# Kernel optimization log

Measured on AMD Instinct MI355X. Metric: run time of the kernel, lower is better.

Reference implementation:

```python
import jax, jax.numpy as jnp
import numpy as np

EPS = 1e-8

def quaternion_normalize(q):
    # q: [..., 4] -> unit quaternion
    return q / (jnp.linalg.norm(q, axis=-1, keepdims=True) + EPS)

def quaternion_mul(q1, q2):
    # Hamilton product; q1, q2 broadcastable [..., 4]
    w1, x1, y1, z1 = q1[..., 0], q1[..., 1], q1[..., 2], q1[..., 3]
    w2, x2, y2, z2 = q2[..., 0], q2[..., 1], q2[..., 2], q2[..., 3]
    w = w1 * w2 - x1 * x2 - y1 * y2 - z1 * z2
    x = w1 * x2 + x1 * w2 + y1 * z2 - z1 * y2
    y = w1 * y2 - x1 * z2 + y1 * w2 + z1 * x2
    z = w1 * z2 + x1 * y2 - y1 * x2 + z1 * w2
    return jnp.stack([w, x, y, z], axis=-1)

def setup_inputs() -> dict:
    key = jax.random.key(0)
    ks = jax.random.split(key, 7)
    B, N, M, D = 2, 512, 512, 256
    return {
        "vision_feat": jax.random.normal(ks[0], (B, N, D), dtype=jnp.float32),
        "text_feat": jax.random.normal(ks[1], (B, M, D), dtype=jnp.float32),
        "Wv": jax.random.normal(ks[2], (D, D), dtype=jnp.float32) * (1.0 / np.sqrt(D)),
        "bv": jax.random.normal(ks[3], (D,), dtype=jnp.float32) * 0.01,
        "Wt": jax.random.normal(ks[4], (D, D), dtype=jnp.float32) * (1.0 / np.sqrt(D)),
        "bt": jax.random.normal(ks[5], (D,), dtype=jnp.float32) * 0.01,
        "h": jnp.float32(1.0),
    }

def reference(vision_feat, text_feat, Wv, bv, Wt, bt, h):
    B, N, D = vision_feat.shape
    M = text_feat.shape[1]
    heads = D // 4
    # project to spinors and normalize per-quaternion
    v_spinor = quaternion_normalize((vision_feat @ Wv.T + bv).reshape(B, N, heads, 4))
    t_spinor = quaternion_normalize((text_feat @ Wt.T + bt).reshape(B, M, heads, 4))
    # broadcast pairwise quaternion product v * conj(t): [B, N, M, heads, 4]
    v_exp = v_spinor[:, :, None]                      # [B, N, 1, heads, 4]
    t_conj = t_spinor[:, None, :] * jnp.array([1.0, -1.0, -1.0, -1.0], dtype=t_spinor.dtype)
    inner = quaternion_mul(v_exp, t_conj)             # [B, N, M, heads, 4]
    vec_norm = jnp.linalg.norm(inner[..., 1:], axis=-1)
    w = inner[..., 0]
    gamma = 2.0 * jnp.arctan2(vec_norm, w + EPS)
    interference = jnp.cos(gamma / 2.0) ** 2          # [B, N, M, heads]
    attn = jax.nn.softmax(interference.mean(axis=-1) / jnp.sqrt(jnp.float32(D)), axis=-1)  # [B, N, M]
    new_vision = jnp.matmul(attn, text_feat)                      # [B, N, D]
    new_text = jnp.matmul(attn.transpose(0, 2, 1), vision_feat)   # [B, M, D]
    out_vision = vision_feat + h * new_vision
    out_text = text_feat + h * new_text
    return (out_vision, out_text)
```

## Files before the change

### kernel.cpp

```cpp
#include <hip/hip_runtime.h>
#include <math.h>

#define EPS 1e-8f

typedef short bf16x8 __attribute__((ext_vector_type(8)));
typedef short bf16x4 __attribute__((ext_vector_type(4)));
typedef float f32x4  __attribute__((ext_vector_type(4)));

__device__ __forceinline__ short f2bf(float f) {
    union { float fv; unsigned u; } v; v.fv = f;
    unsigned r = v.u + 0x7fffu + ((v.u >> 16) & 1u);
    return (short)(r >> 16);
}
__device__ __forceinline__ float bf2f(short s) {
    union { unsigned u; float f; } v;
    v.u = ((unsigned)(unsigned short)s) << 16;
    return v.f;
}
__device__ __forceinline__ bf16x8 pack8(float4 a, float4 b) {
    bf16x8 p;
    p[0] = f2bf(a.x); p[1] = f2bf(a.y); p[2] = f2bf(a.z); p[3] = f2bf(a.w);
    p[4] = f2bf(b.x); p[5] = f2bf(b.y); p[6] = f2bf(b.z); p[7] = f2bf(b.w);
    return p;
}

__global__ __launch_bounds__(256) void proj_expand_kernel(
    const float* __restrict__ vis, const float* __restrict__ txt,
    const float* __restrict__ Wv, const float* __restrict__ bv,
    const float* __restrict__ Wt, const float* __restrict__ bt,
    short* __restrict__ expq)
{
    const int which = blockIdx.z;
    const float* X    = which == 0 ? vis : txt;
    const float* W    = which == 0 ? Wv : Wt;
    const float* bias = which == 0 ? bv : bt;
    short* Eo = expq + which * 1024 * 1024;

    const int r0 = blockIdx.x * 32;
    const int c0 = blockIdx.y * 64;
    const int t = threadIdx.x, lane = t & 63, wave = t >> 6;
    const int wr = (wave >> 1) * 16, wc = (wave & 1) * 32;
    const int mrow = lane & 15, quad = lane >> 4;

    __shared__ __align__(16) short As[32][72];
    __shared__ __align__(16) short Bs[64][72];

    f32x4 acc[2] = {};

    const int srow = t >> 3, skg = t & 7;
    for (int k0 = 0; k0 < 256; k0 += 64) {
        const float* xp = X + (r0 + srow) * 256 + k0 + 8 * skg;
        float4 xa = *(const float4*)xp, xb = *(const float4*)(xp + 4);
        const float* wp0 = W + (c0 + srow) * 256 + k0 + 8 * skg;
        const float* wp1 = W + (c0 + srow + 32) * 256 + k0 + 8 * skg;
        float4 wa0 = *(const float4*)wp0, wb0 = *(const float4*)(wp0 + 4);
        float4 wa1 = *(const float4*)wp1, wb1 = *(const float4*)(wp1 + 4);
        __syncthreads();
        *(bf16x8*)&As[srow][8 * skg]      = pack8(xa, xb);
        *(bf16x8*)&Bs[srow][8 * skg]      = pack8(wa0, wb0);
        *(bf16x8*)&Bs[srow + 32][8 * skg] = pack8(wa1, wb1);
        __syncthreads();
        #pragma unroll
        for (int kh = 0; kh < 2; ++kh) {
            bf16x8 a  = *(bf16x8*)&As[wr + mrow][32 * kh + 8 * quad];
            bf16x8 b0 = *(bf16x8*)&Bs[wc + mrow][32 * kh + 8 * quad];
            bf16x8 b1 = *(bf16x8*)&Bs[wc + 16 + mrow][32 * kh + 8 * quad];
            acc[0] = __builtin_amdgcn_mfma_f32_16x16x32_bf16(a, b0, acc[0], 0, 0, 0);
            acc[1] = __builtin_amdgcn_mfma_f32_16x16x32_bf16(a, b1, acc[1], 0, 0, 0);
        }
    }

    const int qbase = lane & ~3;
    #pragma unroll
    for (int j = 0; j < 2; ++j) {
        const int col  = c0 + wc + 16 * j + mrow;
        const float bb = bias[col];
        const int head = col >> 2;
        #pragma unroll
        for (int reg = 0; reg < 4; ++reg) {
            const int row = r0 + wr + quad * 4 + reg;
            float v = acc[j][reg] + bb;
            float s = v * v;
            s += __shfl_xor(s, 1, 64);
            s += __shfl_xor(s, 2, 64);
            float q = v * (1.f / (sqrtf(s) + EPS));
            float q0 = __shfl(q, qbase + 0, 64);
            float q1 = __shfl(q, qbase + 1, 64);
            float q2 = __shfl(q, qbase + 2, 64);
            float q3 = __shfl(q, qbase + 3, 64);
            bf16x4 p;
            p[0] = f2bf(q * q0); p[1] = f2bf(q * q1);
            p[2] = f2bf(q * q2); p[3] = f2bf(q * q3);
            *(bf16x4*)(Eo + row * 1024 + head * 16 + (col & 3) * 4) = p;
        }
    }
}

__global__ __launch_bounds__(256) void logits_kernel(
    const short* __restrict__ expq, short* __restrict__ E,
    float* __restrict__ rs)
{
    const int b  = blockIdx.z;
    const int r0 = blockIdx.x * 32;
    const int c0 = blockIdx.y * 64;
    const int t = threadIdx.x, lane = t & 63, wave = t >> 6;
    const int wr = (wave >> 1) * 16, wc = (wave & 1) * 32;
    const int mrow = lane & 15, quad = lane >> 4;

    __shared__ __align__(16) short As[32][72];
    __shared__ __align__(16) short Bs[64][72];

    const short* Abase = expq + (b * 512 + r0) * 1024;
    const short* Bbase = expq + (1024 + b * 512 + c0) * 1024;

    f32x4 acc[2] = {};
    const int srow = t >> 3, skg = t & 7;
    for (int k0 = 0; k0 < 1024; k0 += 64) {
        bf16x8 av = *(const bf16x8*)(Abase + srow * 1024 + k0 + 8 * skg);
        bf16x8 b0v = *(const bf16x8*)(Bbase + srow * 1024 + k0 + 8 * skg);
        bf16x8 b1v = *(const bf16x8*)(Bbase + (srow + 32) * 1024 + k0 + 8 * skg);
        __syncthreads();
        *(bf16x8*)&As[srow][8 * skg]      = av;
        *(bf16x8*)&Bs[srow][8 * skg]      = b0v;
        *(bf16x8*)&Bs[srow + 32][8 * skg] = b1v;
        __syncthreads();
        #pragma unroll
        for (int kh = 0; kh < 2; ++kh) {
            bf16x8 a  = *(bf16x8*)&As[wr + mrow][32 * kh + 8 * quad];
            bf16x8 b0 = *(bf16x8*)&Bs[wc + mrow][32 * kh + 8 * quad];
            bf16x8 b1 = *(bf16x8*)&Bs[wc + 16 + mrow][32 * kh + 8 * quad];
            acc[0] = __builtin_amdgcn_mfma_f32_16x16x32_bf16(a, b0, acc[0], 0, 0, 0);
            acc[1] = __builtin_amdgcn_mfma_f32_16x16x32_bf16(a, b1, acc[1], 0, 0, 0);
        }
    }

    float e[2][4];
    #pragma unroll
    for (int j = 0; j < 2; ++j)
        #pragma unroll
        for (int reg = 0; reg < 4; ++reg)
            e[j][reg] = __expf(acc[j][reg] * (1.f / 1024.f));

    #pragma unroll
    for (int j = 0; j < 2; ++j) {
        const int col = c0 + wc + 16 * j + mrow;
        #pragma unroll
        for (int reg = 0; reg < 4; ++reg) {
            const int row = r0 + wr + quad * 4 + reg;
            E[(b * 512 + row) * 512 + col] = f2bf(e[j][reg]);
        }
    }
    #pragma unroll
    for (int reg = 0; reg < 4; ++reg) {
        float p = e[0][reg] + e[1][reg];
        p += __shfl_xor(p, 1, 64);
        p += __shfl_xor(p, 2, 64);
        p += __shfl_xor(p, 4, 64);
        p += __shfl_xor(p, 8, 64);
        if (mrow == 0) {
            const int row = r0 + wr + quad * 4 + reg;
            rs[(b * 512 + row) * 16 + (c0 >> 5) + (wc >> 5)] = p;
        }
    }
}

__global__ __launch_bounds__(256) void out_kernel(
    const float* __restrict__ vis, const float* __restrict__ txt,
    const short* __restrict__ E, const float* __restrict__ rs,
    const float* __restrict__ hptr,
    float* __restrict__ outv, float* __restrict__ outt)
{
    const int z = blockIdx.z;
    const int b = z & 1, which = z >> 1;
    const int r0 = blockIdx.x * 32;
    const int c0 = blockIdx.y * 64;
    const int t = threadIdx.x, lane = t & 63, wave = t >> 6;
    const int wr = (wave >> 1) * 16, wc = (wave & 1) * 32;
    const int mrow = lane & 15, quad = lane >> 4;
    const float hv = hptr[0];

    const short* Eb   = E + b * 512 * 512;
    const float* S    = (which == 0 ? txt : vis) + b * 512 * 256;
    const float* base = (which == 0 ? vis : txt) + b * 512 * 256;
    float*       out  = (which == 0 ? outv : outt) + b * 512 * 256;

    __shared__ __align__(16) short As[32][72];
    __shared__ __align__(16) short Bs[64][72];
    __shared__ float rinv_s[512];

    #pragma unroll
    for (int u = 0; u < 2; ++u) {
        const int row = t + 256 * u;
        const float* p = rs + (b * 512 + row) * 16;
        float s = 0.f;
        #pragma unroll
        for (int i = 0; i < 16; ++i) s += p[i];
        rinv_s[row] = 1.f / s;
    }
    __syncthreads();

    f32x4 acc[2] = {};
    const int kkB = t >> 3, cg = t & 7;
    const int rowA = t >> 3, kgA = t & 7;
    const int nnA = t >> 2, mgA = t & 3;

    for (int k0 = 0; k0 < 512; k0 += 64) {
        float4 sa[2], sb[2];
        #pragma unroll
        for (int u = 0; u < 2; ++u) {
            const float* sp = S + (k0 + kkB + 32 * u) * 256 + c0 + 8 * cg;
            sa[u] = *(const float4*)sp; sb[u] = *(const float4*)(sp + 4);
        }
        bf16x8 arow;
        float af[8];
        if (which == 0) {
            arow = *(const bf16x8*)(Eb + (r0 + rowA) * 512 + k0 + 8 * kgA);
        } else {
            bf16x8 ev = *(const bf16x8*)(Eb + (k0 + nnA) * 512 + r0 + 8 * mgA);
            const float ri = rinv_s[k0 + nnA];
            #pragma unroll
            for (int c = 0; c < 8; ++c) af[c] = bf2f(ev[c]) * ri;
        }
        __syncthreads();
        if (which == 0) {
            *(bf16x8*)&As[rowA][8 * kgA] = arow;
        } else {
            #pragma unroll
            for (int c = 0; c < 8; ++c) As[8 * mgA + c][nnA] = f2bf(af[c]);
        }
        #pragma unroll
        for (int u = 0; u < 2; ++u) {
            const int kk = kkB + 32 * u;
            Bs[8 * cg + 0][kk] = f2bf(sa[u].x);
            Bs[8 * cg + 1][kk] = f2bf(sa[u].y);
            Bs[8 * cg + 2][kk] = f2bf(sa[u].z);
            Bs[8 * cg + 3][kk] = f2bf(sa[u].w);
            Bs[8 * cg + 4][kk] = f2bf(sb[u].x);
            Bs[8 * cg + 5][kk] = f2bf(sb[u].y);
            Bs[8 * cg + 6][kk] = f2bf(sb[u].z);
            Bs[8 * cg + 7][kk] = f2bf(sb[u].w);
        }
        __syncthreads();
        #pragma unroll
        for (int kh = 0; kh < 2; ++kh) {
            bf16x8 a  = *(bf16x8*)&As[wr + mrow][32 * kh + 8 * quad];
            bf16x8 b0 = *(bf16x8*)&Bs[wc + mrow][32 * kh + 8 * quad];
            bf16x8 b1 = *(bf16x8*)&Bs[wc + 16 + mrow][32 * kh + 8 * quad];
            acc[0] = __builtin_amdgcn_mfma_f32_16x16x32_bf16(a, b0, acc[0], 0, 0, 0);
            acc[1] = __builtin_amdgcn_mfma_f32_16x16x32_bf16(a, b1, acc[1], 0, 0, 0);
        }
    }

    #pragma unroll
    for (int j = 0; j < 2; ++j) {
        const int col = c0 + wc + 16 * j + mrow;
        #pragma unroll
        for (int reg = 0; reg < 4; ++reg) {
            const int row = r0 + wr + quad * 4 + reg;
            const float scale = which == 0 ? hv * rinv_s[row] : hv;
            out[row * 256 + col] = fmaf(scale, acc[j][reg], base[row * 256 + col]);
        }
    }
}

extern "C" void kernel_launch(void* const* d_in, const int* in_sizes, int n_in,
                              void* d_out, int out_size, void* d_ws, size_t ws_size,
                              hipStream_t stream)
{
    const float* vis = (const float*)d_in[0];
    const float* txt = (const float*)d_in[1];
    const float* Wv  = (const float*)d_in[2];
    const float* bv  = (const float*)d_in[3];
    const float* Wt  = (const float*)d_in[4];
    const float* bt  = (const float*)d_in[5];
    const float* h   = (const float*)d_in[6];

    float* outv = (float*)d_out;
    float* outt = (float*)d_out + 2 * 512 * 256;

    short* expq = (short*)d_ws;
    short* E    = expq + 2048 * 1024;
    float* rs   = (float*)(E + 1024 * 512);

    proj_expand_kernel<<<dim3(32, 4, 2), 256, 0, stream>>>(vis, txt, Wv, bv, Wt, bt, expq);
    logits_kernel<<<dim3(16, 8, 2), 256, 0, stream>>>(expq, E, rs);
    out_kernel<<<dim3(16, 4, 4), 256, 0, stream>>>(vis, txt, E, rs, h, outv, outt);
}
```

Before: 94.09 us.

## Emit transposed bf16 features in projection kernel; restage expansion epilogue via LDS

The projection kernel now writes a transposed bf16 copy of each input feature tile (taken from its shared-memory A tile) into workspace. The output kernel can then load its B operand with vectorized bf16 loads instead of reading fp32, converting and doing scalar transposed LDS stores. The quaternion outer-product epilogue is also rewritten to stage accumulators through LDS and emit two 16-byte stores per head instead of shuffles and 8-byte stores. This adds workspace traffic and an extra barrier in the projection kernel.

```diff
diff --git a/kernel.cpp b/kernel.cpp
--- a/kernel.cpp
+++ b/kernel.cpp
@@ -4,7 +4,6 @@
 #define EPS 1e-8f
 
 typedef short bf16x8 __attribute__((ext_vector_type(8)));
-typedef short bf16x4 __attribute__((ext_vector_type(4)));
 typedef float f32x4  __attribute__((ext_vector_type(4)));
 
 __device__ __forceinline__ short f2bf(float f) {
@@ -28,7 +27,7 @@
     const float* __restrict__ vis, const float* __restrict__ txt,
     const float* __restrict__ Wv, const float* __restrict__ bv,
     const float* __restrict__ Wt, const float* __restrict__ bt,
-    short* __restrict__ expq)
+    short* __restrict__ expq, short* __restrict__ St)
 {
     const int which = blockIdx.z;
     const float* X    = which == 0 ? vis : txt;
@@ -48,6 +47,8 @@
     f32x4 acc[2] = {};
 
     const int srow = t >> 3, skg = t & 7;
+    const int kexp = 64 * blockIdx.y;
+
     for (int k0 = 0; k0 < 256; k0 += 64) {
         const float* xp = X + (r0 + srow) * 256 + k0 + 8 * skg;
         float4 xa = *(const float4*)xp, xb = *(const float4*)(xp + 4);
@@ -68,31 +69,52 @@
             acc[0] = __builtin_amdgcn_mfma_f32_16x16x32_bf16(a, b0, acc[0], 0, 0, 0);
             acc[1] = __builtin_amdgcn_mfma_f32_16x16x32_bf16(a, b1, acc[1], 0, 0, 0);
         }
-    }
-
-    const int qbase = lane & ~3;
+        if (k0 == kexp) {
+            const int kk = t & 63, rg = t >> 6;
+            bf16x8 p;
+            #pragma unroll
+            for (int i = 0; i < 8; ++i) p[i] = As[8 * rg + i][kk];
+            const int b = r0 >> 9, mb = r0 & 511;
+            *(bf16x8*)(St + which * 262144 + b * 131072 +
+                       (kexp + kk) * 512 + mb + 8 * rg) = p;
+        }
+    }
+
+    __syncthreads();
+    float* fs = (float*)&Bs[0][0];
     #pragma unroll
     for (int j = 0; j < 2; ++j) {
-        const int col  = c0 + wc + 16 * j + mrow;
-        const float bb = bias[col];
-        const int head = col >> 2;
+        const int lcol = wc + 16 * j + mrow;
+        const float bb = bias[c0 + lcol];
         #pragma unroll
         for (int reg = 0; reg < 4; ++reg) {
-            const int row = r0 + wr + quad * 4 + reg;
-            float v = acc[j][reg] + bb;
-            float s = v * v;
-            s += __shfl_xor(s, 1, 64);
-            s += __shfl_xor(s, 2, 64);
-            float q = v * (1.f / (sqrtf(s) + EPS));
-            float q0 = __shfl(q, qbase + 0, 64);
-            float q1 = __shfl(q, qbase + 1, 64);
-            float q2 = __shfl(q, qbase + 2, 64);
-            float q3 = __shfl(q, qbase + 3, 64);
-            bf16x4 p;
-            p[0] = f2bf(q * q0); p[1] = f2bf(q * q1);
-            p[2] = f2bf(q * q2); p[3] = f2bf(q * q3);
-            *(bf16x4*)(Eo + row * 1024 + head * 16 + (col & 3) * 4) = p;
-        }
+            const int lrow = wr + quad * 4 + reg;
+            fs[lrow * 65 + lcol] = acc[j][reg] + bb;
+        }
+    }
+    __syncthreads();
+    #pragma unroll
+    for (int u = 0; u < 2; ++u) {
+        const int qid = t + 256 * u;
+        const int lrow = qid >> 4, lhq = qid & 15;
+        const float* qp = fs + lrow * 65 + 4 * lhq;
+        float q0 = qp[0], q1 = qp[1], q2 = qp[2], q3 = qp[3];
+        float s = q0 * q0 + q1 * q1 + q2 * q2 + q3 * q3;
+        float inv = 1.f / (sqrtf(s) + EPS);
+        q0 *= inv; q1 *= inv; q2 *= inv; q3 *= inv;
+        const float qc[4] = {q0, q1, q2, q3};
+        bf16x8 pa, pb;
+        #pragma unroll
+        for (int i = 0; i < 2; ++i)
+            #pragma unroll
+            for (int jj = 0; jj < 4; ++jj) pa[4 * i + jj] = f2bf(qc[i] * qc[jj]);
+        #pragma unroll
+        for (int i = 0; i < 2; ++i)
+            #pragma unroll
+            for (int jj = 0; jj < 4; ++jj) pb[4 * i + jj] = f2bf(qc[2 + i] * qc[jj]);
+        short* dst = Eo + (r0 + lrow) * 1024 + (16 * blockIdx.y + lhq) * 16;
+        *(bf16x8*)dst       = pa;
+        *(bf16x8*)(dst + 8) = pb;
     }
 }
 
@@ -116,7 +138,7 @@
     f32x4 acc[2] = {};
     const int srow = t >> 3, skg = t & 7;
     for (int k0 = 0; k0 < 1024; k0 += 64) {
-        bf16x8 av = *(const bf16x8*)(Abase + srow * 1024 + k0 + 8 * skg);
+        bf16x8 av  = *(const bf16x8*)(Abase + srow * 1024 + k0 + 8 * skg);
         bf16x8 b0v = *(const bf16x8*)(Bbase + srow * 1024 + k0 + 8 * skg);
         bf16x8 b1v = *(const bf16x8*)(Bbase + (srow + 32) * 1024 + k0 + 8 * skg);
         __syncthreads();
@@ -167,7 +189,7 @@
 __global__ __launch_bounds__(256) void out_kernel(
     const float* __restrict__ vis, const float* __restrict__ txt,
     const short* __restrict__ E, const float* __restrict__ rs,
-    const float* __restrict__ hptr,
+    const short* __restrict__ St, const float* __restrict__ hptr,
     float* __restrict__ outv, float* __restrict__ outt)
 {
     const int z = blockIdx.z;
@@ -180,7 +202,7 @@
     const float hv = hptr[0];
 
     const short* Eb   = E + b * 512 * 512;
-    const float* S    = (which == 0 ? txt : vis) + b * 512 * 256;
+    const short* Sb   = St + (1 - which) * 262144 + b * 131072;
     const float* base = (which == 0 ? vis : txt) + b * 512 * 256;
     float*       out  = (which == 0 ? outv : outt) + b * 512 * 256;
 
@@ -200,17 +222,13 @@
     __syncthreads();
 
     f32x4 acc[2] = {};
-    const int kkB = t >> 3, cg = t & 7;
+    const int cB = t >> 2, kgB = t & 3;
     const int rowA = t >> 3, kgA = t & 7;
     const int nnA = t >> 2, mgA = t & 3;
 
     for (int k0 = 0; k0 < 512; k0 += 64) {
-        float4 sa[2], sb[2];
-        #pragma unroll
-        for (int u = 0; u < 2; ++u) {
-            const float* sp = S + (k0 + kkB + 32 * u) * 256 + c0 + 8 * cg;
-            sa[u] = *(const float4*)sp; sb[u] = *(const float4*)(sp + 4);
-        }
+        bf16x8 sb0 = *(const bf16x8*)(Sb + (c0 + cB) * 512 + k0 + 8 * kgB);
+        bf16x8 sb1 = *(const bf16x8*)(Sb + (c0 + cB) * 512 + k0 + 8 * kgB + 32);
         bf16x8 arow;
         float af[8];
         if (which == 0) {
@@ -228,18 +246,8 @@
             #pragma unroll
             for (int c = 0; c < 8; ++c) As[8 * mgA + c][nnA] = f2bf(af[c]);
         }
-        #pragma unroll
-        for (int u = 0; u < 2; ++u) {
-            const int kk = kkB + 32 * u;
-            Bs[8 * cg + 0][kk] = f2bf(sa[u].x);
-            Bs[8 * cg + 1][kk] = f2bf(sa[u].y);
-            Bs[8 * cg + 2][kk] = f2bf(sa[u].z);
-            Bs[8 * cg + 3][kk] = f2bf(sa[u].w);
-            Bs[8 * cg + 4][kk] = f2bf(sb[u].x);
-            Bs[8 * cg + 5][kk] = f2bf(sb[u].y);
-            Bs[8 * cg + 6][kk] = f2bf(sb[u].z);
-            Bs[8 * cg + 7][kk] = f2bf(sb[u].w);
-        }
+        *(bf16x8*)&Bs[cB][8 * kgB]      = sb0;
+        *(bf16x8*)&Bs[cB][8 * kgB + 32] = sb1;
         __syncthreads();
         #pragma unroll
         for (int kh = 0; kh < 2; ++kh) {
@@ -281,8 +289,9 @@
     short* expq = (short*)d_ws;
     short* E    = expq + 2048 * 1024;
     float* rs   = (float*)(E + 1024 * 512);
-
-    proj_expand_kernel<<<dim3(32, 4, 2), 256, 0, stream>>>(vis, txt, Wv, bv, Wt, bt, expq);
+    short* St   = (short*)(rs + 1024 * 16);
+
+    proj_expand_kernel<<<dim3(32, 4, 2), 256, 0, stream>>>(vis, txt, Wv, bv, Wt, bt, expq, St);
     logits_kernel<<<dim3(16, 8, 2), 256, 0, stream>>>(expq, E, rs);
-    out_kernel<<<dim3(16, 4, 4), 256, 0, stream>>>(vis, txt, E, rs, h, outv, outt);
-}
+    out_kernel<<<dim3(16, 4, 4), 256, 0, stream>>>(vis, txt, E, rs, St, h, outv, outt);
+}
```

Result: slower. 97.00 us (+3.1%).
